# Optimization experiments

Measured on AMD Instinct MI355X. Metric: run time of the kernel, lower is better.

The kernel has to match this reference:

```python
import jax, jax.numpy as jnp
import numpy as np

N = 50000
EH = 500000
ES = 250000
D_IN = 128
D_HID = 128
N_CLS = 47


def _mean_agg(feat, src, dst, n):
    # gather src features, scatter-mean onto dst (DGL copy_u + mean)
    msg = feat[src]                                   # [E, d]
    s = jax.ops.segment_sum(msg, dst, num_segments=n)  # [N, d]
    cnt = jax.ops.segment_sum(jnp.ones((src.shape[0],), feat.dtype), dst, num_segments=n)
    return s / jnp.maximum(cnt, 1.0)[:, None]


def _sage_cv_layer(H, HBar, W, b, hs, hd, ss, sd):
    hbar_new = _mean_agg(HBar, hs, hd, N)             # history etype
    hdelta_new = _mean_agg(H - HBar, ss, sd, N)       # sampled etype
    h_neigh = hbar_new + hdelta_new
    z = jnp.concatenate([H, h_neigh], axis=1)         # [N, 2*d_in]
    return jax.nn.relu(z @ W.T + b)


def setup_inputs() -> dict:
    key = jax.random.key(0)
    ks = jax.random.split(key, 16)
    gain = float(np.sqrt(2.0))  # calculate_gain('relu')

    def xavier(k, shape):
        fan_out, fan_in = shape
        a = gain * np.sqrt(6.0 / (fan_in + fan_out))
        return jax.random.uniform(k, shape, jnp.float32, -a, a)

    return {
        "x": jax.random.normal(ks[0], (N, D_IN), jnp.float32),
        "hbar0": jax.random.normal(ks[1], (N, D_IN), jnp.float32),
        "hbar1": jax.random.normal(ks[2], (N, D_HID), jnp.float32),
        "W0": xavier(ks[3], (D_HID, 2 * D_IN)),
        "b0": jnp.zeros((D_HID,), jnp.float32),
        "W1": xavier(ks[4], (N_CLS, 2 * D_HID)),
        "b1": jnp.zeros((N_CLS,), jnp.float32),
        "hist_src0": jax.random.randint(ks[5], (EH,), 0, N),
        "hist_dst0": jax.random.randint(ks[6], (EH,), 0, N),
        "samp_src0": jax.random.randint(ks[7], (ES,), 0, N),
        "samp_dst0": jax.random.randint(ks[8], (ES,), 0, N),
        "hist_src1": jax.random.randint(ks[9], (EH,), 0, N),
        "hist_dst1": jax.random.randint(ks[10], (EH,), 0, N),
        "samp_src1": jax.random.randint(ks[11], (ES,), 0, N),
        "samp_dst1": jax.random.randint(ks[12], (ES,), 0, N),
    }


def reference(x, hbar0, hbar1, W0, b0, W1, b1,
              hist_src0, hist_dst0, samp_src0, samp_dst0,
              hist_src1, hist_dst1, samp_src1, samp_dst1):
    h = _sage_cv_layer(x, hbar0, W0, b0, hist_src0, hist_dst0, samp_src0, samp_dst0)
    h = _sage_cv_layer(h, hbar1, W1, b1, hist_src1, hist_dst1, samp_src1, samp_dst1)
    return h  # [N, n_classes]
```

## Files before the change

### kernel.cpp

```cpp
#include <hip/hip_runtime.h>

#define D_FEAT 128
#define K_DIM  256
#define EPB 4096
#define PADL 136


typedef __attribute__((ext_vector_type(8))) short bf16x8;
typedef __attribute__((ext_vector_type(4))) float f32x4;
typedef __attribute__((ext_vector_type(2))) float f32x2;

__device__ __forceinline__ unsigned short f2b(float f) {
    union { float f; unsigned u; } cv; cv.f = f;
    return (unsigned short)((cv.u + 0x7fffu + ((cv.u >> 16) & 1u)) >> 16);
}

__device__ __forceinline__ unsigned pack2(float lo, float hi) {
    return (unsigned)f2b(lo) | ((unsigned)f2b(hi) << 16);
}

__device__ __forceinline__ uint4 pack8(float4 a, float4 b) {
    return make_uint4(pack2(a.x, a.y), pack2(a.z, a.w), pack2(b.x, b.y), pack2(b.z, b.w));
}

__device__ __forceinline__ f32x2 up2(unsigned u) {
    union { unsigned u; float f; } lo, hi;
    lo.u = u << 16; hi.u = u & 0xffff0000u;
    f32x2 r; r.x = lo.f; r.y = hi.f; return r;
}

__device__ __forceinline__ void addu4p(f32x2* a, uint4 v) {
    a[0] += up2(v.x); a[1] += up2(v.y); a[2] += up2(v.z); a[3] += up2(v.w);
}

__device__ __forceinline__ float blo(unsigned u) { union { unsigned u; float f; } c; c.u = u << 16; return c.f; }
__device__ __forceinline__ float bhi(unsigned u) { union { unsigned u; float f; } c; c.u = u & 0xffff0000u; return c.f; }

__device__ __forceinline__ long yoff(int y, int EH, int ES) {
    return (long)((y + 1) >> 1) * EH + (long)(y >> 1) * ES;
}


__global__ __launch_bounds__(256)
void histB(const int* __restrict__ hd0, const int* __restrict__ sd0,
           const int* __restrict__ hd1, const int* __restrict__ sd1,
           int EH, int ES, int* __restrict__ bucketCnt, int nb2) {
    int y = blockIdx.y;
    const int* d = (y == 0) ? hd0 : (y == 1) ? sd0 : (y == 2) ? hd1 : sd1;
    int E = (y & 1) ? ES : EH;
    __shared__ int cnt[256];
    int t = threadIdx.x;
    cnt[t] = 0;
    __syncthreads();
    int i0 = blockIdx.x * EPB;
    #pragma unroll
    for (int j = 0; j < 16; ++j) {
        int i = i0 + j * 256 + t;
        if (i < E) atomicAdd(&cnt[d[i] >> 8], 1);
    }
    __syncthreads();
    if (t < nb2 && cnt[t] > 0) atomicAdd(&bucketCnt[y * nb2 + t], cnt[t]);
}

__global__ __launch_bounds__(256)
void scanBuckets(const int* __restrict__ bucketCnt, int* __restrict__ rpBucket,
                 int* __restrict__ bcur, int nb2) {
    int y = blockIdx.x;
    int t = threadIdx.x;
    __shared__ int sh[256];
    int c = (t < nb2) ? bucketCnt[y * nb2 + t] : 0;
    sh[t] = c;
    __syncthreads();
    for (int o = 1; o < 256; o <<= 1) {
        int x = (t >= o) ? sh[t - o] : 0;
        __syncthreads();
        sh[t] += x;
        __syncthreads();
    }
    int excl = t ? sh[t - 1] : 0;
    if (t < nb2) {
        rpBucket[y * (nb2 + 1) + t] = excl;
        bcur[y * nb2 + t] = excl;
    }
    if (t == 0) rpBucket[y * (nb2 + 1) + nb2] = sh[255];
}

__global__ __launch_bounds__(256)
void binA(const int* __restrict__ hs0, const int* __restrict__ hd0,
          const int* __restrict__ ss0, const int* __restrict__ sd0,
          const int* __restrict__ hs1, const int* __restrict__ hd1,
          const int* __restrict__ ss1, const int* __restrict__ sd1,
          int EH, int ES, int* __restrict__ bcur, unsigned* __restrict__ recs,
          int nb2) {
    int y = blockIdx.y;
    const int* src = (y == 0) ? hs0 : (y == 1) ? ss0 : (y == 2) ? hs1 : ss1;
    const int* dst = (y == 0) ? hd0 : (y == 1) ? sd0 : (y == 2) ? hd1 : sd1;
    int E = (y & 1) ? ES : EH;
    unsigned* rb = recs + yoff(y, EH, ES);

    __shared__ int cnt[256];
    int t = threadIdx.x;
    cnt[t] = 0;
    __syncthreads();
    int i0 = blockIdx.x * EPB;
    #pragma unroll
    for (int j = 0; j < 16; ++j) {
        int i = i0 + j * 256 + t;
        if (i < E) atomicAdd(&cnt[dst[i] >> 8], 1);
    }
    __syncthreads();
    int c = cnt[t];
    __syncthreads();
    if (t < nb2 && c > 0) cnt[t] = atomicAdd(&bcur[y * nb2 + t], c);
    __syncthreads();
    #pragma unroll
    for (int j = 0; j < 16; ++j) {
        int i = i0 + j * 256 + t;
        if (i < E) {
            int dd = dst[i];
            int slot = atomicAdd(&cnt[dd >> 8], 1);
            rb[slot] = (unsigned)src[i] | ((unsigned)(dd & 255) << 24);
        }
    }
}

__global__ __launch_bounds__(256)
void placeB(const unsigned* __restrict__ recs, const int* __restrict__ rpBucket,
            int* __restrict__ rpAll, int* __restrict__ srcAll,
            int EH, int ES, int n, int nb2) {
    int y = blockIdx.y;
    int b = blockIdx.x;
    int E = (y & 1) ? ES : EH;
    int* rp = rpAll + (size_t)y * (n + 1);
    long off = yoff(y, EH, ES);
    const unsigned* rb = recs + off;
    int* sb = srcAll + off;
    int e0 = rpBucket[y * (nb2 + 1) + b];
    int e1 = rpBucket[y * (nb2 + 1) + b + 1];
    int nodeBase = b << 8;

    __shared__ int cnt[256];
    __shared__ int sh[256];
    int t = threadIdx.x;
    cnt[t] = 0;
    __syncthreads();
    for (int e = e0 + t; e < e1; e += 256)
        atomicAdd(&cnt[rb[e] >> 24], 1);
    __syncthreads();
    sh[t] = cnt[t];
    __syncthreads();
    for (int o = 1; o < 256; o <<= 1) {
        int x = (t >= o) ? sh[t - o] : 0;
        __syncthreads();
        sh[t] += x;
        __syncthreads();
    }
    int base = e0 + (t ? sh[t - 1] : 0);
    if (nodeBase + t < n) rp[nodeBase + t] = base;
    if (b == 0 && t == 0) rp[n] = E;
    cnt[t] = base;
    __syncthreads();
    for (int e = e0 + t; e < e1; e += 256) {
        unsigned r = rb[e];
        int p = atomicAdd(&cnt[r >> 24], 1);
        sb[p] = (int)(r & 0x00FFFFFFu);
    }
}

__global__ __launch_bounds__(256)
void prep_static(const float4* __restrict__ x, const float4* __restrict__ hbar0,
                 const float4* __restrict__ hbar1,
                 uint4* __restrict__ hb0, uint4* __restrict__ db0,
                 uint4* __restrict__ hb1, uint4* __restrict__ z, int n16) {
    int i = blockIdx.x * 256 + threadIdx.x;
    if (i >= n16) return;
    float4 xa = x[i * 2],     xb = x[i * 2 + 1];
    float4 ba = hbar0[i * 2], bb = hbar0[i * 2 + 1];
    float4 ca = hbar1[i * 2], cb = hbar1[i * 2 + 1];
    hb0[i] = pack8(ba, bb);
    db0[i] = pack8(make_float4(xa.x - ba.x, xa.y - ba.y, xa.z - ba.z, xa.w - ba.w),
                   make_float4(xb.x - bb.x, xb.y - bb.y, xb.z - bb.z, xb.w - bb.w));
    hb1[i] = pack8(ca, cb);
    int g = i >> 4, seg = i & 15;
    int G = g >> 4, r = g & 15, k0 = seg >> 2, kq = seg & 3;
    z[((size_t)G * 8 + k0) * 64 + kq * 16 + r] = pack8(xa, xb);
}

__global__ __launch_bounds__(256)
void conv_weights(const float* __restrict__ W0, unsigned short* __restrict__ WbF0,
                  const float* __restrict__ W1, unsigned short* __restrict__ WbF1) {
    int i = blockIdx.x * 256 + threadIdx.x;
    if (i < 4096) {
        int k0 = i >> 9, T = (i >> 6) & 7, lane = i & 63;
        int col = T * 16 + (lane & 15);
        int kb = k0 * 32 + (lane >> 4) * 8;
        const float* src = W0 + (size_t)col * 256 + kb;
        unsigned short* dst = WbF0 + (size_t)i * 8;
        #pragma unroll
        for (int e = 0; e < 8; ++e) dst[e] = f2b(src[e]);
    }
    if (i < 1536) {
        int k0 = i / 192, rem = i % 192;
        int T = rem >> 6, lane = rem & 63;
        int col = T * 16 + (lane & 15);
        int kb = k0 * 32 + (lane >> 4) * 8;
        unsigned short* dst = WbF1 + (size_t)i * 8;
        #pragma unroll
        for (int e = 0; e < 8; ++e)
            dst[e] = (col < 47) ? f2b(W1[(size_t)col * 256 + kb + e]) : (unsigned short)0;
    }
}

__global__ __launch_bounds__(256)
void aggregate_z(const uint4* __restrict__ HB, const uint4* __restrict__ DB,
                 const int* __restrict__ rpH, const int* __restrict__ srcH,
                 const int* __restrict__ rpS, const int* __restrict__ srcS,
                 uint4* __restrict__ z, int n) {
    int g = blockIdx.x * 4 + (threadIdx.x >> 6);
    if (g >= n) return;
    int lane = threadIdx.x & 63;
    int j = lane >> 4, l = lane & 15;

    int hb_ = rpH[g], he = rpH[g + 1];
    int sb  = rpS[g], se = rpS[g + 1];
    int dH = he - hb_, dS = se - sb;
    int nIt = max((dH + 7) >> 3, (dS + 7) >> 3);

    f32x2 a[4] = {};
    f32x2 d[4] = {};

    int iH1 = hb_ + j, iH2 = hb_ + 4 + j;
    int iS1 = sb + j,  iS2 = sb + 4 + j;
    int sH1 = 0, sH2 = 0, sS1 = 0, sS2 = 0;
    if (iH1 < he) sH1 = srcH[iH1];
    if (iH2 < he) sH2 = srcH[iH2];
    if (iS1 < se) sS1 = srcS[iS1];
    if (iS2 < se) sS2 = srcS[iS2];

    for (int it = 0; it < nIt; ++it) {
        uint4 h1 = make_uint4(0, 0, 0, 0), h2 = make_uint4(0, 0, 0, 0);
        uint4 s1 = make_uint4(0, 0, 0, 0), s2 = make_uint4(0, 0, 0, 0);
        if (iH1 < he) h1 = HB[(size_t)sH1 * 16 + l];
        if (iH2 < he) h2 = HB[(size_t)sH2 * 16 + l];
        if (iS1 < se) s1 = DB[(size_t)sS1 * 16 + l];
        if (iS2 < se) s2 = DB[(size_t)sS2 * 16 + l];
        iH1 += 8; iH2 += 8; iS1 += 8; iS2 += 8;
        if (iH1 < he) sH1 = srcH[iH1];
        if (iH2 < he) sH2 = srcH[iH2];
        if (iS1 < se) sS1 = srcS[iS1];
        if (iS2 < se) sS2 = srcS[iS2];
        addu4p(a, h1); addu4p(a, h2);
        addu4p(d, s1); addu4p(d, s2);
    }

    float rH = 1.0f / fmaxf((float)dH, 1.0f);
    float rS = 1.0f / fmaxf((float)dS, 1.0f);
    float s[8];
    #pragma unroll
    for (int i = 0; i < 4; ++i) {
        float v0 = a[i].x * rH + d[i].x * rS;
        float v1 = a[i].y * rH + d[i].y * rS;
        v0 += __shfl_xor(v0, 16);
        v0 += __shfl_xor(v0, 32);
        v1 += __shfl_xor(v1, 16);
        v1 += __shfl_xor(v1, 32);
        s[2 * i] = v0;
        s[2 * i + 1] = v1;
    }
    if (j == 0) {
        uint4 rv = make_uint4(pack2(s[0], s[1]), pack2(s[2], s[3]),
                              pack2(s[4], s[5]), pack2(s[6], s[7]));
        size_t slot = ((size_t)(g >> 4) * 8 + 4 + (l >> 2)) * 64 + (l & 3) * 16 + (g & 15);
        z[slot] = rv;
    }
}

__global__ __launch_bounds__(256, 2)
void gemm_mfma_l0(const unsigned short* __restrict__ Z, const unsigned short* __restrict__ Wb,
                  const float* __restrict__ bias, const float* __restrict__ hbar1,
                  unsigned short* __restrict__ db1, unsigned short* __restrict__ zl, int n) {
    __shared__ unsigned short hl[32 * PADL];
    int tid  = threadIdx.x;
    int wave = tid >> 6;
    int lane = tid & 63;
    int rt = wave >> 1;
    int ch = wave & 1;
    int m0 = blockIdx.x * 32;
    int cl = lane & 15;
    int kq = lane >> 4;

    const short* Af = (const short*)Z;
    const short* Bf = (const short*)Wb;
    size_t G = (size_t)(m0 >> 4) + rt;

    bf16x8 aF[8];
    #pragma unroll
    for (int k0 = 0; k0 < 8; ++k0)
        aF[k0] = *(const bf16x8*)(Af + ((G * 8 + k0) * 64 + lane) * 8);

    f32x4 acc[4] = {};
    bf16x8 bF[2][4];
    #pragma unroll
    for (int t = 0; t < 4; ++t)
        bF[0][t] = *(const bf16x8*)(Bf + ((size_t)((0 * 8 + ch * 4 + t)) * 64 + lane) * 8);

    #pragma unroll
    for (int k0 = 0; k0 < 8; ++k0) {
        int cur = k0 & 1, nxt = cur ^ 1;
        if (k0 < 7) {
            #pragma unroll
            for (int t = 0; t < 4; ++t)
                bF[nxt][t] = *(const bf16x8*)(Bf + ((size_t)(((k0 + 1) * 8 + ch * 4 + t)) * 64 + lane) * 8);
        }
        #pragma unroll
        for (int t = 0; t < 4; ++t)
            acc[t] = __builtin_amdgcn_mfma_f32_16x16x32_bf16(aF[k0], bF[cur][t], acc[t], 0, 0, 0);
    }

    #pragma unroll
    for (int t = 0; t < 4; ++t) {
        int c = ch * 64 + t * 16 + cl;
        float bv = bias[c];
        #pragma unroll
        for (int r = 0; r < 4; ++r) {
            int row = rt * 16 + kq * 4 + r;
            hl[row * PADL + c] = f2b(fmaxf(acc[t][r] + bv, 0.0f));
        }
    }
    __syncthreads();

    #pragma unroll
    for (int s = 0; s < 2; ++s) {
        int ls = tid + s * 256;
        int gi = ls >> 8, k0 = (ls >> 6) & 3, ln = ls & 63;
        int rl = gi * 16 + (ln & 15);
        int col = k0 * 32 + (ln >> 4) * 8;
        int m = m0 + rl;
        if (m < n) {
            uint4 v = *(const uint4*)(hl + rl * PADL + col);
            ((uint4*)zl)[((size_t)(m0 >> 4) + gi) * 8 * 64 + (size_t)k0 * 64 + ln] = v;
        }
    }

    int row  = tid >> 3;
    int col  = (tid & 7) * 16;
    int m    = m0 + row;
    if (m < n) {
        const uint4* hr = (const uint4*)(hl + row * PADL + col);
        uint4 v0 = hr[0];
        uint4 v1 = hr[1];
        const float4* hb = (const float4*)(hbar1 + (size_t)m * 128 + col);
        float4 h0 = hb[0], h1 = hb[1], h2 = hb[2], h3 = hb[3];
        uint4 d0, d1;
        d0.x = pack2(blo(v0.x) - h0.x, bhi(v0.x) - h0.y);
        d0.y = pack2(blo(v0.y) - h0.z, bhi(v0.y) - h0.w);
        d0.z = pack2(blo(v0.z) - h1.x, bhi(v0.z) - h1.y);
        d0.w = pack2(blo(v0.w) - h1.z, bhi(v0.w) - h1.w);
        d1.x = pack2(blo(v1.x) - h2.x, bhi(v1.x) - h2.y);
        d1.y = pack2(blo(v1.y) - h2.z, bhi(v1.y) - h2.w);
        d1.z = pack2(blo(v1.z) - h3.x, bhi(v1.z) - h3.y);
        d1.w = pack2(blo(v1.w) - h3.z, bhi(v1.w) - h3.w);
        uint4* dp = (uint4*)(db1 + (size_t)m * 128 + col);
        dp[0] = d0;
        dp[1] = d1;
    }
}

template<int NT>
__global__ __launch_bounds__(128, 2)
void gemm_mfma(const unsigned short* __restrict__ Z, const unsigned short* __restrict__ Wb,
               const float* __restrict__ bias, float* __restrict__ out, int n, int COLS) {
    int wave = threadIdx.x >> 6;
    int lane = threadIdx.x & 63;
    int m0 = blockIdx.x * 32 + wave * 16;
    int cl = lane & 15;
    int kq = lane >> 4;

    const short* Af = (const short*)Z;
    const short* Bf = (const short*)Wb;
    size_t G = (size_t)(m0 >> 4);

    bf16x8 aF[8];
    #pragma unroll
    for (int k0 = 0; k0 < 8; ++k0)
        aF[k0] = *(const bf16x8*)(Af + ((G * 8 + k0) * 64 + lane) * 8);

    f32x4 acc[NT] = {};
    bf16x8 bF[2][NT];
    #pragma unroll
    for (int t = 0; t < NT; ++t)
        bF[0][t] = *(const bf16x8*)(Bf + ((size_t)(0 * NT + t) * 64 + lane) * 8);

    #pragma unroll
    for (int k0 = 0; k0 < 8; ++k0) {
        int cur = k0 & 1, nxt = cur ^ 1;
        if (k0 < 7) {
            #pragma unroll
            for (int t = 0; t < NT; ++t)
                bF[nxt][t] = *(const bf16x8*)(Bf + ((size_t)((k0 + 1) * NT + t) * 64 + lane) * 8);
        }
        #pragma unroll
        for (int t = 0; t < NT; ++t)
            acc[t] = __builtin_amdgcn_mfma_f32_16x16x32_bf16(aF[k0], bF[cur][t], acc[t], 0, 0, 0);
    }

    int rg = kq * 4;
    #pragma unroll
    for (int t = 0; t < NT; ++t) {
        int c = t * 16 + cl;
        if (c >= COLS) continue;
        float bv = bias[c];
        #pragma unroll
        for (int r = 0; r < 4; ++r) {
            int m = m0 + rg + r;
            if (m < n) out[(size_t)m * COLS + c] = fmaxf(acc[t][r] + bv, 0.f);
        }
    }
}

extern "C" void kernel_launch(void* const* d_in, const int* in_sizes, int n_in,
                              void* d_out, int out_size, void* d_ws, size_t ws_size,
                              hipStream_t stream) {
    const float* x     = (const float*)d_in[0];
    const float* hbar0 = (const float*)d_in[1];
    const float* hbar1 = (const float*)d_in[2];
    const float* W0    = (const float*)d_in[3];
    const float* b0    = (const float*)d_in[4];
    const float* W1    = (const float*)d_in[5];
    const float* b1    = (const float*)d_in[6];
    const int* hs0 = (const int*)d_in[7];
    const int* hd0 = (const int*)d_in[8];
    const int* ss0 = (const int*)d_in[9];
    const int* sd0 = (const int*)d_in[10];
    const int* hs1 = (const int*)d_in[11];
    const int* hd1 = (const int*)d_in[12];
    const int* ss1 = (const int*)d_in[13];
    const int* sd1 = (const int*)d_in[14];

    const int n   = in_sizes[0] / D_FEAT;
    const int EH  = in_sizes[7];
    const int ES  = in_sizes[9];
    const int nb2 = (n + 255) / 256;

    int* bucketCnt = (int*)d_ws;
    int* rpBucket  = bucketCnt + 4 * nb2;
    int* bcur      = rpBucket + 4 * (nb2 + 1);
    int* rpAll     = bcur + 4 * nb2;
    int* srcAll    = rpAll + 4 * (size_t)(n + 1);
    unsigned* recs = (unsigned*)(srcAll + 2 * (size_t)EH + 2 * (size_t)ES);
    size_t int_words = (size_t)12 * nb2 + 4 + 4 * (size_t)(n + 1)
                     + 4 * (size_t)EH + 4 * (size_t)ES;
    int_words = (int_words + 3) & ~(size_t)3;
    unsigned short* hb0 = (unsigned short*)((int*)d_ws + int_words);
    unsigned short* db0 = hb0 + (size_t)n * D_FEAT;
    unsigned short* hb1 = db0 + (size_t)n * D_FEAT;
    unsigned short* db1 = hb1 + (size_t)n * D_FEAT;
    unsigned short* z   = db1 + (size_t)n * D_FEAT;
    unsigned short* Wb0 = z + (size_t)n * K_DIM + 4096;
    unsigned short* Wb1 = Wb0 + 128 * 256;

    const int* rpH0 = rpAll;
    const int* rpS0 = rpAll + (size_t)(n + 1);
    const int* rpH1 = rpAll + 2 * (size_t)(n + 1);
    const int* rpS1 = rpAll + 3 * (size_t)(n + 1);
    int* srcH0 = srcAll;
    int* srcS0 = srcAll + (size_t)EH;
    int* srcH1 = srcAll + (size_t)EH + ES;
    int* srcS1 = srcAll + 2 * (size_t)EH + ES;

    dim3 blk(256);
    int binb  = (EH + EPB - 1) / EPB;
    int prepb = ((n * 16) + 255) / 256;
    int aggb  = (n + 3) / 4;
    int gemmb0 = (n + 31) / 32;
    int gemmb1 = (n + 31) / 32;

    hipMemsetAsync(bucketCnt, 0, 4 * (size_t)nb2 * sizeof(int), stream);
    conv_weights<<<16, blk, 0, stream>>>(W0, Wb0, W1, Wb1);
    histB<<<dim3(binb, 4), blk, 0, stream>>>(hd0, sd0, hd1, sd1, EH, ES, bucketCnt, nb2);
    scanBuckets<<<4, blk, 0, stream>>>(bucketCnt, rpBucket, bcur, nb2);
    binA<<<dim3(binb, 4), blk, 0, stream>>>(hs0, hd0, ss0, sd0, hs1, hd1, ss1, sd1,
                                            EH, ES, bcur, recs, nb2);
    placeB<<<dim3(nb2, 4), blk, 0, stream>>>(recs, rpBucket, rpAll, srcAll, EH, ES, n, nb2);
    prep_static<<<prepb, blk, 0, stream>>>((const float4*)x, (const float4*)hbar0,
                                           (const float4*)hbar1, (uint4*)hb0, (uint4*)db0,
                                           (uint4*)hb1, (uint4*)z, n * 16);

    aggregate_z<<<aggb, blk, 0, stream>>>((const uint4*)hb0, (const uint4*)db0,
                                          rpH0, srcH0, rpS0, srcS0, (uint4*)z, n);
    gemm_mfma_l0<<<gemmb0, blk, 0, stream>>>(z, Wb0, b0, hbar1, db1, z, n);

    aggregate_z<<<aggb, blk, 0, stream>>>((const uint4*)hb1, (const uint4*)db1,
                                          rpH1, srcH1, rpS1, srcS1, (uint4*)z, n);
    gemm_mfma<3><<<gemmb1, dim3(128), 0, stream>>>(z, Wb1, b1, (float*)d_out, n, 47);
}
```

Baseline: 300.5 us.

## Hoist layer-1 history aggregation into layer-0 aggregation launch

Layer 1's history-edge mean aggregation depends only on hbar1, not on layer 0's output. It is now computed in the same launch as layer 0's aggregation, using a second set of blocks, and written to a new bf16 buffer hm1. The layer-1 aggregation then gathers only sampled edges and adds hm1 in. History gathers also go 16 edges per iteration instead of 8 to increase memory-level parallelism. The trade-off is an extra intermediate buffer write and read, plus an extra bf16 rounding of the history mean.

Result: slower. 315.1 us (+4.9%).

```diff
diff --git a/kernel.cpp b/kernel.cpp
--- a/kernel.cpp
+++ b/kernel.cpp
@@ -212,54 +212,166 @@
 }
 
 __global__ __launch_bounds__(256)
-void aggregate_z(const uint4* __restrict__ HB, const uint4* __restrict__ DB,
-                 const int* __restrict__ rpH, const int* __restrict__ srcH,
-                 const int* __restrict__ rpS, const int* __restrict__ srcS,
-                 uint4* __restrict__ z, int n) {
+void agg_l0_h1(const uint4* __restrict__ HB0, const uint4* __restrict__ DB0,
+               const int* __restrict__ rpH0, const int* __restrict__ srcH0,
+               const int* __restrict__ rpS0, const int* __restrict__ srcS0,
+               uint4* __restrict__ z,
+               const uint4* __restrict__ HB1, const int* __restrict__ rpH1,
+               const int* __restrict__ srcH1, uint4* __restrict__ hm1,
+               int n, int nblk0) {
+    int lane = threadIdx.x & 63;
+    int j = lane >> 4, l = lane & 15;
+
+    if ((int)blockIdx.x < nblk0) {
+        int g = blockIdx.x * 4 + (threadIdx.x >> 6);
+        if (g >= n) return;
+        int hb_ = rpH0[g], he = rpH0[g + 1];
+        int sb  = rpS0[g], se = rpS0[g + 1];
+        int dH = he - hb_, dS = se - sb;
+        int nH = (dH + 15) >> 4, nS = (dS + 7) >> 3;
+        int nIt = nH > nS ? nH : nS;
+
+        f32x2 a[4] = {};
+        f32x2 d[4] = {};
+
+        int iH1 = hb_ + j, iH2 = hb_ + 4 + j, iH3 = hb_ + 8 + j, iH4 = hb_ + 12 + j;
+        int iS1 = sb + j,  iS2 = sb + 4 + j;
+        int sH1 = 0, sH2 = 0, sH3 = 0, sH4 = 0, sS1 = 0, sS2 = 0;
+        if (iH1 < he) sH1 = srcH0[iH1];
+        if (iH2 < he) sH2 = srcH0[iH2];
+        if (iH3 < he) sH3 = srcH0[iH3];
+        if (iH4 < he) sH4 = srcH0[iH4];
+        if (iS1 < se) sS1 = srcS0[iS1];
+        if (iS2 < se) sS2 = srcS0[iS2];
+
+        for (int it = 0; it < nIt; ++it) {
+            uint4 h1 = make_uint4(0,0,0,0), h2 = make_uint4(0,0,0,0);
+            uint4 h3 = make_uint4(0,0,0,0), h4 = make_uint4(0,0,0,0);
+            uint4 s1 = make_uint4(0,0,0,0), s2 = make_uint4(0,0,0,0);
+            if (iH1 < he) h1 = HB0[(size_t)sH1 * 16 + l];
+            if (iH2 < he) h2 = HB0[(size_t)sH2 * 16 + l];
+            if (iH3 < he) h3 = HB0[(size_t)sH3 * 16 + l];
+            if (iH4 < he) h4 = HB0[(size_t)sH4 * 16 + l];
+            if (iS1 < se) s1 = DB0[(size_t)sS1 * 16 + l];
+            if (iS2 < se) s2 = DB0[(size_t)sS2 * 16 + l];
+            iH1 += 16; iH2 += 16; iH3 += 16; iH4 += 16;
+            iS1 += 8;  iS2 += 8;
+            if (iH1 < he) sH1 = srcH0[iH1];
+            if (iH2 < he) sH2 = srcH0[iH2];
+            if (iH3 < he) sH3 = srcH0[iH3];
+            if (iH4 < he) sH4 = srcH0[iH4];
+            if (iS1 < se) sS1 = srcS0[iS1];
+            if (iS2 < se) sS2 = srcS0[iS2];
+            addu4p(a, h1); addu4p(a, h2); addu4p(a, h3); addu4p(a, h4);
+            addu4p(d, s1); addu4p(d, s2);
+        }
+
+        float rH = 1.0f / fmaxf((float)dH, 1.0f);
+        float rS = 1.0f / fmaxf((float)dS, 1.0f);
+        float s[8];
+        #pragma unroll
+        for (int i = 0; i < 4; ++i) {
+            float v0 = a[i].x * rH + d[i].x * rS;
+            float v1 = a[i].y * rH + d[i].y * rS;
+            v0 += __shfl_xor(v0, 16);
+            v0 += __shfl_xor(v0, 32);
+            v1 += __shfl_xor(v1, 16);
+            v1 += __shfl_xor(v1, 32);
+            s[2 * i] = v0;
+            s[2 * i + 1] = v1;
+        }
+        if (j == 0) {
+            uint4 rv = make_uint4(pack2(s[0], s[1]), pack2(s[2], s[3]),
+                                  pack2(s[4], s[5]), pack2(s[6], s[7]));
+            size_t slot = ((size_t)(g >> 4) * 8 + 4 + (l >> 2)) * 64 + (l & 3) * 16 + (g & 15);
+            z[slot] = rv;
+        }
+    } else {
+        int g = ((int)blockIdx.x - nblk0) * 4 + (threadIdx.x >> 6);
+        if (g >= n) return;
+        int hb_ = rpH1[g], he = rpH1[g + 1];
+        int dH = he - hb_;
+        int nIt = (dH + 15) >> 4;
+
+        f32x2 a[4] = {};
+        int iH1 = hb_ + j, iH2 = hb_ + 4 + j, iH3 = hb_ + 8 + j, iH4 = hb_ + 12 + j;
+        int sH1 = 0, sH2 = 0, sH3 = 0, sH4 = 0;
+        if (iH1 < he) sH1 = srcH1[iH1];
+        if (iH2 < he) sH2 = srcH1[iH2];
+        if (iH3 < he) sH3 = srcH1[iH3];
+        if (iH4 < he) sH4 = srcH1[iH4];
+
+        for (int it = 0; it < nIt; ++it) {
+            uint4 h1 = make_uint4(0,0,0,0), h2 = make_uint4(0,0,0,0);
+            uint4 h3 = make_uint4(0,0,0,0), h4 = make_uint4(0,0,0,0);
+            if (iH1 < he) h1 = HB1[(size_t)sH1 * 16 + l];
+            if (iH2 < he) h2 = HB1[(size_t)sH2 * 16 + l];
+            if (iH3 < he) h3 = HB1[(size_t)sH3 * 16 + l];
+            if (iH4 < he) h4 = HB1[(size_t)sH4 * 16 + l];
+            iH1 += 16; iH2 += 16; iH3 += 16; iH4 += 16;
+            if (iH1 < he) sH1 = srcH1[iH1];
+            if (iH2 < he) sH2 = srcH1[iH2];
+            if (iH3 < he) sH3 = srcH1[iH3];
+            if (iH4 < he) sH4 = srcH1[iH4];
+            addu4p(a, h1); addu4p(a, h2); addu4p(a, h3); addu4p(a, h4);
+        }
+
+        float rH = 1.0f / fmaxf((float)dH, 1.0f);
+        float s[8];
+        #pragma unroll
+        for (int i = 0; i < 4; ++i) {
+            float v0 = a[i].x * rH;
+            float v1 = a[i].y * rH;
+            v0 += __shfl_xor(v0, 16);
+            v0 += __shfl_xor(v0, 32);
+            v1 += __shfl_xor(v1, 16);
+            v1 += __shfl_xor(v1, 32);
+            s[2 * i] = v0;
+            s[2 * i + 1] = v1;
+        }
+        if (j == 0) {
+            uint4 rv = make_uint4(pack2(s[0], s[1]), pack2(s[2], s[3]),
+                                  pack2(s[4], s[5]), pack2(s[6], s[7]));
+            hm1[(size_t)g * 16 + l] = rv;
+        }
+    }
+}
+
+__global__ __launch_bounds__(256)
+void agg_s1(const uint4* __restrict__ DB1, const int* __restrict__ rpS,
+            const int* __restrict__ srcS, const uint4* __restrict__ hm1,
+            uint4* __restrict__ z, int n) {
     int g = blockIdx.x * 4 + (threadIdx.x >> 6);
     if (g >= n) return;
     int lane = threadIdx.x & 63;
     int j = lane >> 4, l = lane & 15;
 
-    int hb_ = rpH[g], he = rpH[g + 1];
-    int sb  = rpS[g], se = rpS[g + 1];
-    int dH = he - hb_, dS = se - sb;
-    int nIt = max((dH + 7) >> 3, (dS + 7) >> 3);
-
-    f32x2 a[4] = {};
+    int sb = rpS[g], se = rpS[g + 1];
+    int dS = se - sb;
+    int nIt = (dS + 7) >> 3;
+
     f32x2 d[4] = {};
-
-    int iH1 = hb_ + j, iH2 = hb_ + 4 + j;
-    int iS1 = sb + j,  iS2 = sb + 4 + j;
-    int sH1 = 0, sH2 = 0, sS1 = 0, sS2 = 0;
-    if (iH1 < he) sH1 = srcH[iH1];
-    if (iH2 < he) sH2 = srcH[iH2];
+    int iS1 = sb + j, iS2 = sb + 4 + j;
+    int sS1 = 0, sS2 = 0;
     if (iS1 < se) sS1 = srcS[iS1];
     if (iS2 < se) sS2 = srcS[iS2];
 
     for (int it = 0; it < nIt; ++it) {
-        uint4 h1 = make_uint4(0, 0, 0, 0), h2 = make_uint4(0, 0, 0, 0);
-        uint4 s1 = make_uint4(0, 0, 0, 0), s2 = make_uint4(0, 0, 0, 0);
-        if (iH1 < he) h1 = HB[(size_t)sH1 * 16 + l];
-        if (iH2 < he) h2 = HB[(size_t)sH2 * 16 + l];
-        if (iS1 < se) s1 = DB[(size_t)sS1 * 16 + l];
-        if (iS2 < se) s2 = DB[(size_t)sS2 * 16 + l];
-        iH1 += 8; iH2 += 8; iS1 += 8; iS2 += 8;
-        if (iH1 < he) sH1 = srcH[iH1];
-        if (iH2 < he) sH2 = srcH[iH2];
+        uint4 s1 = make_uint4(0,0,0,0), s2 = make_uint4(0,0,0,0);
+        if (iS1 < se) s1 = DB1[(size_t)sS1 * 16 + l];
+        if (iS2 < se) s2 = DB1[(size_t)sS2 * 16 + l];
+        iS1 += 8; iS2 += 8;
         if (iS1 < se) sS1 = srcS[iS1];
         if (iS2 < se) sS2 = srcS[iS2];
-        addu4p(a, h1); addu4p(a, h2);
         addu4p(d, s1); addu4p(d, s2);
     }
 
-    float rH = 1.0f / fmaxf((float)dH, 1.0f);
     float rS = 1.0f / fmaxf((float)dS, 1.0f);
     float s[8];
     #pragma unroll
     for (int i = 0; i < 4; ++i) {
-        float v0 = a[i].x * rH + d[i].x * rS;
-        float v1 = a[i].y * rH + d[i].y * rS;
+        float v0 = d[i].x * rS;
+        float v1 = d[i].y * rS;
         v0 += __shfl_xor(v0, 16);
         v0 += __shfl_xor(v0, 32);
         v1 += __shfl_xor(v1, 16);
@@ -268,6 +380,11 @@
         s[2 * i + 1] = v1;
     }
     if (j == 0) {
+        uint4 hm = hm1[(size_t)g * 16 + l];
+        s[0] += blo(hm.x); s[1] += bhi(hm.x);
+        s[2] += blo(hm.y); s[3] += bhi(hm.y);
+        s[4] += blo(hm.z); s[5] += bhi(hm.z);
+        s[6] += blo(hm.w); s[7] += bhi(hm.w);
         uint4 rv = make_uint4(pack2(s[0], s[1]), pack2(s[2], s[3]),
                               pack2(s[4], s[5]), pack2(s[6], s[7]));
         size_t slot = ((size_t)(g >> 4) * 8 + 4 + (l >> 2)) * 64 + (l & 3) * 16 + (g & 15);
@@ -458,6 +575,7 @@
     unsigned short* z   = db1 + (size_t)n * D_FEAT;
     unsigned short* Wb0 = z + (size_t)n * K_DIM + 4096;
     unsigned short* Wb1 = Wb0 + 128 * 256;
+    unsigned short* hm1 = Wb1 + 64 * 256;
 
     const int* rpH0 = rpAll;
     const int* rpS0 = rpAll + (size_t)(n + 1);
@@ -486,11 +604,13 @@
                                            (const float4*)hbar1, (uint4*)hb0, (uint4*)db0,
                                            (uint4*)hb1, (uint4*)z, n * 16);
 
-    aggregate_z<<<aggb, blk, 0, stream>>>((const uint4*)hb0, (const uint4*)db0,
-                                          rpH0, srcH0, rpS0, srcS0, (uint4*)z, n);
+    agg_l0_h1<<<2 * aggb, blk, 0, stream>>>((const uint4*)hb0, (const uint4*)db0,
+                                            rpH0, srcH0, rpS0, srcS0, (uint4*)z,
+                                            (const uint4*)hb1, rpH1, srcH1, (uint4*)hm1,
+                                            n, aggb);
     gemm_mfma_l0<<<gemmb0, blk, 0, stream>>>(z, Wb0, b0, hbar1, db1, z, n);
 
-    aggregate_z<<<aggb, blk, 0, stream>>>((const uint4*)hb1, (const uint4*)db1,
-                                          rpH1, srcH1, rpS1, srcS1, (uint4*)z, n);
+    agg_s1<<<aggb, blk, 0, stream>>>((const uint4*)db1, rpS1, srcS1, (const uint4*)hm1,
+                                     (uint4*)z, n);
     gemm_mfma<3><<<gemmb1, dim3(128), 0, stream>>>(z, Wb1, b1, (float*)d_out, n, 47);
 }
```

## Replace two-level bucket CSR build with per-node global-atomic counting sort

Applied to the files above, without the earlier changes.

Replaces the bucketed histogram/bin/place CSR construction with a direct per-node count using global atomics, a two-level scan (per-block, then across blocks), a base fix-up, and a single scatter pass with global atomic cursors. It also fuses feature prep, weight conversion and the degree histogram into one launch. The aim is fewer kernel launches and no intermediate packed-record pass. In exchange it relies on contended global atomics, and the edge order within a node's list is no longer deterministic.

Result: slower. 395.2 us (+31.5%).

```diff
diff --git a/kernel.cpp b/kernel.cpp
--- a/kernel.cpp
+++ b/kernel.cpp
@@ -40,174 +40,137 @@
     return (long)((y + 1) >> 1) * EH + (long)(y >> 1) * ES;
 }
 
-
-__global__ __launch_bounds__(256)
-void histB(const int* __restrict__ hd0, const int* __restrict__ sd0,
-           const int* __restrict__ hd1, const int* __restrict__ sd1,
-           int EH, int ES, int* __restrict__ bucketCnt, int nb2) {
-    int y = blockIdx.y;
-    const int* d = (y == 0) ? hd0 : (y == 1) ? sd0 : (y == 2) ? hd1 : sd1;
-    int E = (y & 1) ? ES : EH;
-    __shared__ int cnt[256];
+__global__ __launch_bounds__(256)
+void head(const float4* __restrict__ x, const float4* __restrict__ hbar0,
+          const float4* __restrict__ hbar1,
+          uint4* __restrict__ hb0, uint4* __restrict__ db0,
+          uint4* __restrict__ hb1, uint4* __restrict__ z, int n16,
+          const float* __restrict__ W0, unsigned short* __restrict__ WbF0,
+          const float* __restrict__ W1, unsigned short* __restrict__ WbF1,
+          const int* __restrict__ hd0, const int* __restrict__ sd0,
+          const int* __restrict__ hd1, const int* __restrict__ sd1,
+          int EH, int ES, int* __restrict__ cnt, int n, int prepb, int binb) {
+    int bid = blockIdx.x;
     int t = threadIdx.x;
-    cnt[t] = 0;
-    __syncthreads();
-    int i0 = blockIdx.x * EPB;
-    #pragma unroll
-    for (int j = 0; j < 16; ++j) {
-        int i = i0 + j * 256 + t;
-        if (i < E) atomicAdd(&cnt[d[i] >> 8], 1);
-    }
-    __syncthreads();
-    if (t < nb2 && cnt[t] > 0) atomicAdd(&bucketCnt[y * nb2 + t], cnt[t]);
-}
-
-__global__ __launch_bounds__(256)
-void scanBuckets(const int* __restrict__ bucketCnt, int* __restrict__ rpBucket,
-                 int* __restrict__ bcur, int nb2) {
-    int y = blockIdx.x;
-    int t = threadIdx.x;
+    if (bid < prepb) {
+        int i = bid * 256 + t;
+        if (i >= n16) return;
+        float4 xa = x[i * 2],     xb = x[i * 2 + 1];
+        float4 ba = hbar0[i * 2], bb = hbar0[i * 2 + 1];
+        float4 ca = hbar1[i * 2], cb = hbar1[i * 2 + 1];
+        hb0[i] = pack8(ba, bb);
+        db0[i] = pack8(make_float4(xa.x - ba.x, xa.y - ba.y, xa.z - ba.z, xa.w - ba.w),
+                       make_float4(xb.x - bb.x, xb.y - bb.y, xb.z - bb.z, xb.w - bb.w));
+        hb1[i] = pack8(ca, cb);
+        int g = i >> 4, seg = i & 15;
+        int G = g >> 4, r = g & 15, k0 = seg >> 2, kq = seg & 3;
+        z[((size_t)G * 8 + k0) * 64 + kq * 16 + r] = pack8(xa, xb);
+    } else if (bid < prepb + 16) {
+        int i = (bid - prepb) * 256 + t;
+        if (i < 4096) {
+            int k0 = i >> 9, T = (i >> 6) & 7, lane = i & 63;
+            int col = T * 16 + (lane & 15);
+            int kb = k0 * 32 + (lane >> 4) * 8;
+            const float* src = W0 + (size_t)col * 256 + kb;
+            unsigned short* dst = WbF0 + (size_t)i * 8;
+            #pragma unroll
+            for (int e = 0; e < 8; ++e) dst[e] = f2b(src[e]);
+        }
+        if (i < 1536) {
+            int k0 = i / 192, rem = i % 192;
+            int T = rem >> 6, lane = rem & 63;
+            int col = T * 16 + (lane & 15);
+            int kb = k0 * 32 + (lane >> 4) * 8;
+            unsigned short* dst = WbF1 + (size_t)i * 8;
+            #pragma unroll
+            for (int e = 0; e < 8; ++e)
+                dst[e] = (col < 47) ? f2b(W1[(size_t)col * 256 + kb + e]) : (unsigned short)0;
+        }
+    } else {
+        int r = bid - prepb - 16;
+        int y = r / binb, c = r % binb;
+        const int* d = (y == 0) ? hd0 : (y == 1) ? sd0 : (y == 2) ? hd1 : sd1;
+        int E = (y & 1) ? ES : EH;
+        int* cn = cnt + (size_t)y * n;
+        int i0 = c * EPB;
+        #pragma unroll
+        for (int j = 0; j < 16; ++j) {
+            int i = i0 + j * 256 + t;
+            if (i < E) atomicAdd(&cn[d[i]], 1);
+        }
+    }
+}
+
+__global__ __launch_bounds__(256)
+void scanN(const int* __restrict__ cnt, int* __restrict__ rpAll,
+           int* __restrict__ bucketSum, int n, int nb2) {
+    int y = blockIdx.y, b = blockIdx.x, t = threadIdx.x;
+    int node = b * 256 + t;
     __shared__ int sh[256];
-    int c = (t < nb2) ? bucketCnt[y * nb2 + t] : 0;
+    int c = (node < n) ? cnt[(size_t)y * n + node] : 0;
     sh[t] = c;
     __syncthreads();
     for (int o = 1; o < 256; o <<= 1) {
-        int x = (t >= o) ? sh[t - o] : 0;
+        int v = (t >= o) ? sh[t - o] : 0;
         __syncthreads();
-        sh[t] += x;
+        sh[t] += v;
         __syncthreads();
     }
-    int excl = t ? sh[t - 1] : 0;
-    if (t < nb2) {
-        rpBucket[y * (nb2 + 1) + t] = excl;
-        bcur[y * nb2 + t] = excl;
-    }
-    if (t == 0) rpBucket[y * (nb2 + 1) + nb2] = sh[255];
-}
-
-__global__ __launch_bounds__(256)
-void binA(const int* __restrict__ hs0, const int* __restrict__ hd0,
-          const int* __restrict__ ss0, const int* __restrict__ sd0,
-          const int* __restrict__ hs1, const int* __restrict__ hd1,
-          const int* __restrict__ ss1, const int* __restrict__ sd1,
-          int EH, int ES, int* __restrict__ bcur, unsigned* __restrict__ recs,
-          int nb2) {
+    if (node < n) rpAll[(size_t)y * (n + 1) + node] = sh[t] - c;
+    if (t == 255) bucketSum[y * nb2 + b] = sh[255];
+}
+
+__global__ __launch_bounds__(256)
+void scanB(const int* __restrict__ bucketSum, int* __restrict__ rpBucket, int nb2) {
+    int y = blockIdx.x, t = threadIdx.x;
+    __shared__ int sh[256];
+    int c = (t < nb2) ? bucketSum[y * nb2 + t] : 0;
+    sh[t] = c;
+    __syncthreads();
+    for (int o = 1; o < 256; o <<= 1) {
+        int v = (t >= o) ? sh[t - o] : 0;
+        __syncthreads();
+        sh[t] += v;
+        __syncthreads();
+    }
+    if (t < nb2) rpBucket[y * (nb2 + 1) + t] = sh[t] - c;
+}
+
+__global__ __launch_bounds__(256)
+void baseFix(int* __restrict__ rpAll, int* __restrict__ cur,
+             const int* __restrict__ rpBucket, int n, int nb2, int EH, int ES) {
+    int y = blockIdx.y;
+    int node = blockIdx.x * 256 + threadIdx.x;
+    if (node < n) {
+        int v = rpAll[(size_t)y * (n + 1) + node] + rpBucket[y * (nb2 + 1) + (node >> 8)];
+        rpAll[(size_t)y * (n + 1) + node] = v;
+        cur[(size_t)y * n + node] = v;
+    }
+    if (blockIdx.x == 0 && threadIdx.x == 0)
+        rpAll[(size_t)y * (n + 1) + n] = (y & 1) ? ES : EH;
+}
+
+__global__ __launch_bounds__(256)
+void scatterE(const int* __restrict__ hs0, const int* __restrict__ hd0,
+              const int* __restrict__ ss0, const int* __restrict__ sd0,
+              const int* __restrict__ hs1, const int* __restrict__ hd1,
+              const int* __restrict__ ss1, const int* __restrict__ sd1,
+              int EH, int ES, int* __restrict__ cur, int* __restrict__ srcAll, int n) {
     int y = blockIdx.y;
     const int* src = (y == 0) ? hs0 : (y == 1) ? ss0 : (y == 2) ? hs1 : ss1;
     const int* dst = (y == 0) ? hd0 : (y == 1) ? sd0 : (y == 2) ? hd1 : sd1;
     int E = (y & 1) ? ES : EH;
-    unsigned* rb = recs + yoff(y, EH, ES);
-
-    __shared__ int cnt[256];
+    int* cn = cur + (size_t)y * n;
+    int* sb = srcAll + yoff(y, EH, ES);
     int t = threadIdx.x;
-    cnt[t] = 0;
-    __syncthreads();
     int i0 = blockIdx.x * EPB;
-    #pragma unroll
-    for (int j = 0; j < 16; ++j) {
-        int i = i0 + j * 256 + t;
-        if (i < E) atomicAdd(&cnt[dst[i] >> 8], 1);
-    }
-    __syncthreads();
-    int c = cnt[t];
-    __syncthreads();
-    if (t < nb2 && c > 0) cnt[t] = atomicAdd(&bcur[y * nb2 + t], c);
-    __syncthreads();
     #pragma unroll
     for (int j = 0; j < 16; ++j) {
         int i = i0 + j * 256 + t;
         if (i < E) {
-            int dd = dst[i];
-            int slot = atomicAdd(&cnt[dd >> 8], 1);
-            rb[slot] = (unsigned)src[i] | ((unsigned)(dd & 255) << 24);
-        }
-    }
-}
-
-__global__ __launch_bounds__(256)
-void placeB(const unsigned* __restrict__ recs, const int* __restrict__ rpBucket,
-            int* __restrict__ rpAll, int* __restrict__ srcAll,
-            int EH, int ES, int n, int nb2) {
-    int y = blockIdx.y;
-    int b = blockIdx.x;
-    int E = (y & 1) ? ES : EH;
-    int* rp = rpAll + (size_t)y * (n + 1);
-    long off = yoff(y, EH, ES);
-    const unsigned* rb = recs + off;
-    int* sb = srcAll + off;
-    int e0 = rpBucket[y * (nb2 + 1) + b];
-    int e1 = rpBucket[y * (nb2 + 1) + b + 1];
-    int nodeBase = b << 8;
-
-    __shared__ int cnt[256];
-    __shared__ int sh[256];
-    int t = threadIdx.x;
-    cnt[t] = 0;
-    __syncthreads();
-    for (int e = e0 + t; e < e1; e += 256)
-        atomicAdd(&cnt[rb[e] >> 24], 1);
-    __syncthreads();
-    sh[t] = cnt[t];
-    __syncthreads();
-    for (int o = 1; o < 256; o <<= 1) {
-        int x = (t >= o) ? sh[t - o] : 0;
-        __syncthreads();
-        sh[t] += x;
-        __syncthreads();
-    }
-    int base = e0 + (t ? sh[t - 1] : 0);
-    if (nodeBase + t < n) rp[nodeBase + t] = base;
-    if (b == 0 && t == 0) rp[n] = E;
-    cnt[t] = base;
-    __syncthreads();
-    for (int e = e0 + t; e < e1; e += 256) {
-        unsigned r = rb[e];
-        int p = atomicAdd(&cnt[r >> 24], 1);
-        sb[p] = (int)(r & 0x00FFFFFFu);
-    }
-}
-
-__global__ __launch_bounds__(256)
-void prep_static(const float4* __restrict__ x, const float4* __restrict__ hbar0,
-                 const float4* __restrict__ hbar1,
-                 uint4* __restrict__ hb0, uint4* __restrict__ db0,
-                 uint4* __restrict__ hb1, uint4* __restrict__ z, int n16) {
-    int i = blockIdx.x * 256 + threadIdx.x;
-    if (i >= n16) return;
-    float4 xa = x[i * 2],     xb = x[i * 2 + 1];
-    float4 ba = hbar0[i * 2], bb = hbar0[i * 2 + 1];
-    float4 ca = hbar1[i * 2], cb = hbar1[i * 2 + 1];
-    hb0[i] = pack8(ba, bb);
-    db0[i] = pack8(make_float4(xa.x - ba.x, xa.y - ba.y, xa.z - ba.z, xa.w - ba.w),
-                   make_float4(xb.x - bb.x, xb.y - bb.y, xb.z - bb.z, xb.w - bb.w));
-    hb1[i] = pack8(ca, cb);
-    int g = i >> 4, seg = i & 15;
-    int G = g >> 4, r = g & 15, k0 = seg >> 2, kq = seg & 3;
-    z[((size_t)G * 8 + k0) * 64 + kq * 16 + r] = pack8(xa, xb);
-}
-
-__global__ __launch_bounds__(256)
-void conv_weights(const float* __restrict__ W0, unsigned short* __restrict__ WbF0,
-                  const float* __restrict__ W1, unsigned short* __restrict__ WbF1) {
-    int i = blockIdx.x * 256 + threadIdx.x;
-    if (i < 4096) {
-        int k0 = i >> 9, T = (i >> 6) & 7, lane = i & 63;
-        int col = T * 16 + (lane & 15);
-        int kb = k0 * 32 + (lane >> 4) * 8;
-        const float* src = W0 + (size_t)col * 256 + kb;
-        unsigned short* dst = WbF0 + (size_t)i * 8;
-        #pragma unroll
-        for (int e = 0; e < 8; ++e) dst[e] = f2b(src[e]);
-    }
-    if (i < 1536) {
-        int k0 = i / 192, rem = i % 192;
-        int T = rem >> 6, lane = rem & 63;
-        int col = T * 16 + (lane & 15);
-        int kb = k0 * 32 + (lane >> 4) * 8;
-        unsigned short* dst = WbF1 + (size_t)i * 8;
-        #pragma unroll
-        for (int e = 0; e < 8; ++e)
-            dst[e] = (col < 47) ? f2b(W1[(size_t)col * 256 + kb + e]) : (unsigned short)0;
+            int slot = atomicAdd(&cn[dst[i]], 1);
+            sb[slot] = src[i];
+        }
     }
 }
 
@@ -442,14 +405,14 @@
     const int ES  = in_sizes[9];
     const int nb2 = (n + 255) / 256;
 
-    int* bucketCnt = (int*)d_ws;
-    int* rpBucket  = bucketCnt + 4 * nb2;
-    int* bcur      = rpBucket + 4 * (nb2 + 1);
-    int* rpAll     = bcur + 4 * nb2;
+    int* cnt       = (int*)d_ws;
+    int* cur       = cnt + 4 * (size_t)n;
+    int* bucketSum = cur + 4 * (size_t)n;
+    int* rpBucket  = bucketSum + 4 * nb2;
+    int* rpAll     = rpBucket + 4 * (nb2 + 1);
     int* srcAll    = rpAll + 4 * (size_t)(n + 1);
-    unsigned* recs = (unsigned*)(srcAll + 2 * (size_t)EH + 2 * (size_t)ES);
-    size_t int_words = (size_t)12 * nb2 + 4 + 4 * (size_t)(n + 1)
-                     + 4 * (size_t)EH + 4 * (size_t)ES;
+    size_t int_words = 8 * (size_t)n + 4 * nb2 + 4 * (nb2 + 1) + 4 * (size_t)(n + 1)
+                     + 2 * (size_t)EH + 2 * (size_t)ES;
     int_words = (int_words + 3) & ~(size_t)3;
     unsigned short* hb0 = (unsigned short*)((int*)d_ws + int_words);
     unsigned short* db0 = hb0 + (size_t)n * D_FEAT;
@@ -475,16 +438,16 @@
     int gemmb0 = (n + 31) / 32;
     int gemmb1 = (n + 31) / 32;
 
-    hipMemsetAsync(bucketCnt, 0, 4 * (size_t)nb2 * sizeof(int), stream);
-    conv_weights<<<16, blk, 0, stream>>>(W0, Wb0, W1, Wb1);
-    histB<<<dim3(binb, 4), blk, 0, stream>>>(hd0, sd0, hd1, sd1, EH, ES, bucketCnt, nb2);
-    scanBuckets<<<4, blk, 0, stream>>>(bucketCnt, rpBucket, bcur, nb2);
-    binA<<<dim3(binb, 4), blk, 0, stream>>>(hs0, hd0, ss0, sd0, hs1, hd1, ss1, sd1,
-                                            EH, ES, bcur, recs, nb2);
-    placeB<<<dim3(nb2, 4), blk, 0, stream>>>(recs, rpBucket, rpAll, srcAll, EH, ES, n, nb2);
-    prep_static<<<prepb, blk, 0, stream>>>((const float4*)x, (const float4*)hbar0,
-                                           (const float4*)hbar1, (uint4*)hb0, (uint4*)db0,
-                                           (uint4*)hb1, (uint4*)z, n * 16);
+    hipMemsetAsync(cnt, 0, 4 * (size_t)n * sizeof(int), stream);
+    head<<<prepb + 16 + 4 * binb, blk, 0, stream>>>(
+        (const float4*)x, (const float4*)hbar0, (const float4*)hbar1,
+        (uint4*)hb0, (uint4*)db0, (uint4*)hb1, (uint4*)z, n * 16,
+        W0, Wb0, W1, Wb1, hd0, sd0, hd1, sd1, EH, ES, cnt, n, prepb, binb);
+    scanN<<<dim3(nb2, 4), blk, 0, stream>>>(cnt, rpAll, bucketSum, n, nb2);
+    scanB<<<4, blk, 0, stream>>>(bucketSum, rpBucket, nb2);
+    baseFix<<<dim3(nb2, 4), blk, 0, stream>>>(rpAll, cur, rpBucket, n, nb2, EH, ES);
+    scatterE<<<dim3(binb, 4), blk, 0, stream>>>(hs0, hd0, ss0, sd0, hs1, hd1, ss1, sd1,
+                                                EH, ES, cur, srcAll, n);
 
     aggregate_z<<<aggb, blk, 0, stream>>>((const uint4*)hb0, (const uint4*)db0,
                                           rpH0, srcH0, rpS0, srcS0, (uint4*)z, n);
```

## Merge binning, feature prep and weight conversion into one launch; cache bucket records in LDS

Applied to the files above, without the earlier changes.

Combines binA, prep_static and conv_weights into a single heterogeneous kernel that dispatches work by block index, removing two launches and letting the memory-bound prep work overlap with edge binning. placeB now keeps each bucket's records in a 16KB shared buffer during the counting pass and reads them back from there when scattering, so the second global read of the records is avoided. The extra shared memory in placeB may lower occupancy, and buckets with more than PB_CAP records still read the overflow from global memory.

New measurement: 291.9 us. 1.03x faster.

```diff
diff --git a/kernel.cpp b/kernel.cpp
--- a/kernel.cpp
+++ b/kernel.cpp
@@ -4,6 +4,7 @@
 #define K_DIM  256
 #define EPB 4096
 #define PADL 136
+#define PB_CAP 4096
 
 
 typedef __attribute__((ext_vector_type(8))) short bf16x8;
@@ -86,40 +87,84 @@
 }
 
 __global__ __launch_bounds__(256)
-void binA(const int* __restrict__ hs0, const int* __restrict__ hd0,
-          const int* __restrict__ ss0, const int* __restrict__ sd0,
-          const int* __restrict__ hs1, const int* __restrict__ hd1,
-          const int* __restrict__ ss1, const int* __restrict__ sd1,
-          int EH, int ES, int* __restrict__ bcur, unsigned* __restrict__ recs,
-          int nb2) {
-    int y = blockIdx.y;
-    const int* src = (y == 0) ? hs0 : (y == 1) ? ss0 : (y == 2) ? hs1 : ss1;
-    const int* dst = (y == 0) ? hd0 : (y == 1) ? sd0 : (y == 2) ? hd1 : sd1;
-    int E = (y & 1) ? ES : EH;
-    unsigned* rb = recs + yoff(y, EH, ES);
-
+void binPrep(const int* __restrict__ hs0, const int* __restrict__ hd0,
+             const int* __restrict__ ss0, const int* __restrict__ sd0,
+             const int* __restrict__ hs1, const int* __restrict__ hd1,
+             const int* __restrict__ ss1, const int* __restrict__ sd1,
+             int EH, int ES, int* __restrict__ bcur, unsigned* __restrict__ recs,
+             int nb2, int binb,
+             const float4* __restrict__ x, const float4* __restrict__ hbar0,
+             const float4* __restrict__ hbar1,
+             uint4* __restrict__ hb0, uint4* __restrict__ db0,
+             uint4* __restrict__ hb1, uint4* __restrict__ z, int n16, int prepb,
+             const float* __restrict__ W0, unsigned short* __restrict__ WbF0,
+             const float* __restrict__ W1, unsigned short* __restrict__ WbF1) {
     __shared__ int cnt[256];
+    int bid = blockIdx.x;
     int t = threadIdx.x;
-    cnt[t] = 0;
-    __syncthreads();
-    int i0 = blockIdx.x * EPB;
-    #pragma unroll
-    for (int j = 0; j < 16; ++j) {
-        int i = i0 + j * 256 + t;
-        if (i < E) atomicAdd(&cnt[dst[i] >> 8], 1);
-    }
-    __syncthreads();
-    int c = cnt[t];
-    __syncthreads();
-    if (t < nb2 && c > 0) cnt[t] = atomicAdd(&bcur[y * nb2 + t], c);
-    __syncthreads();
-    #pragma unroll
-    for (int j = 0; j < 16; ++j) {
-        int i = i0 + j * 256 + t;
-        if (i < E) {
-            int dd = dst[i];
-            int slot = atomicAdd(&cnt[dd >> 8], 1);
-            rb[slot] = (unsigned)src[i] | ((unsigned)(dd & 255) << 24);
+
+    if (bid < 4 * binb) {
+        int y = bid / binb, c = bid % binb;
+        const int* src = (y == 0) ? hs0 : (y == 1) ? ss0 : (y == 2) ? hs1 : ss1;
+        const int* dst = (y == 0) ? hd0 : (y == 1) ? sd0 : (y == 2) ? hd1 : sd1;
+        int E = (y & 1) ? ES : EH;
+        unsigned* rb = recs + yoff(y, EH, ES);
+
+        cnt[t] = 0;
+        __syncthreads();
+        int i0 = c * EPB;
+        #pragma unroll
+        for (int j = 0; j < 16; ++j) {
+            int i = i0 + j * 256 + t;
+            if (i < E) atomicAdd(&cnt[dst[i] >> 8], 1);
+        }
+        __syncthreads();
+        int cc = cnt[t];
+        __syncthreads();
+        if (t < nb2 && cc > 0) cnt[t] = atomicAdd(&bcur[y * nb2 + t], cc);
+        __syncthreads();
+        #pragma unroll
+        for (int j = 0; j < 16; ++j) {
+            int i = i0 + j * 256 + t;
+            if (i < E) {
+                int dd = dst[i];
+                int slot = atomicAdd(&cnt[dd >> 8], 1);
+                rb[slot] = (unsigned)src[i] | ((unsigned)(dd & 255) << 24);
+            }
+        }
+    } else if (bid < 4 * binb + prepb) {
+        int i = (bid - 4 * binb) * 256 + t;
+        if (i >= n16) return;
+        float4 xa = x[i * 2],     xb = x[i * 2 + 1];
+        float4 ba = hbar0[i * 2], bb = hbar0[i * 2 + 1];
+        float4 ca = hbar1[i * 2], cb = hbar1[i * 2 + 1];
+        hb0[i] = pack8(ba, bb);
+        db0[i] = pack8(make_float4(xa.x - ba.x, xa.y - ba.y, xa.z - ba.z, xa.w - ba.w),
+                       make_float4(xb.x - bb.x, xb.y - bb.y, xb.z - bb.z, xb.w - bb.w));
+        hb1[i] = pack8(ca, cb);
+        int g = i >> 4, seg = i & 15;
+        int G = g >> 4, r = g & 15, k0 = seg >> 2, kq = seg & 3;
+        z[((size_t)G * 8 + k0) * 64 + kq * 16 + r] = pack8(xa, xb);
+    } else {
+        int i = (bid - 4 * binb - prepb) * 256 + t;
+        if (i < 4096) {
+            int k0 = i >> 9, T = (i >> 6) & 7, lane = i & 63;
+            int col = T * 16 + (lane & 15);
+            int kb = k0 * 32 + (lane >> 4) * 8;
+            const float* src = W0 + (size_t)col * 256 + kb;
+            unsigned short* dst = WbF0 + (size_t)i * 8;
+            #pragma unroll
+            for (int e = 0; e < 8; ++e) dst[e] = f2b(src[e]);
+        }
+        if (i < 1536) {
+            int k0 = i / 192, rem = i % 192;
+            int T = rem >> 6, lane = rem & 63;
+            int col = T * 16 + (lane & 15);
+            int kb = k0 * 32 + (lane >> 4) * 8;
+            unsigned short* dst = WbF1 + (size_t)i * 8;
+            #pragma unroll
+            for (int e = 0; e < 8; ++e)
+                dst[e] = (col < 47) ? f2b(W1[(size_t)col * 256 + kb + e]) : (unsigned short)0;
         }
     }
 }
@@ -138,21 +183,26 @@
     int e0 = rpBucket[y * (nb2 + 1) + b];
     int e1 = rpBucket[y * (nb2 + 1) + b + 1];
     int nodeBase = b << 8;
-
+    int ne = e1 - e0;
+
+    __shared__ unsigned eb[PB_CAP];
     __shared__ int cnt[256];
     __shared__ int sh[256];
     int t = threadIdx.x;
     cnt[t] = 0;
     __syncthreads();
-    for (int e = e0 + t; e < e1; e += 256)
-        atomicAdd(&cnt[rb[e] >> 24], 1);
+    for (int e = t; e < ne; e += 256) {
+        unsigned r = rb[e0 + e];
+        if (e < PB_CAP) eb[e] = r;
+        atomicAdd(&cnt[r >> 24], 1);
+    }
     __syncthreads();
     sh[t] = cnt[t];
     __syncthreads();
     for (int o = 1; o < 256; o <<= 1) {
-        int x = (t >= o) ? sh[t - o] : 0;
-        __syncthreads();
-        sh[t] += x;
+        int v = (t >= o) ? sh[t - o] : 0;
+        __syncthreads();
+        sh[t] += v;
         __syncthreads();
     }
     int base = e0 + (t ? sh[t - 1] : 0);
@@ -160,54 +210,10 @@
     if (b == 0 && t == 0) rp[n] = E;
     cnt[t] = base;
     __syncthreads();
-    for (int e = e0 + t; e < e1; e += 256) {
-        unsigned r = rb[e];
+    for (int e = t; e < ne; e += 256) {
+        unsigned r = (e < PB_CAP) ? eb[e] : rb[e0 + e];
         int p = atomicAdd(&cnt[r >> 24], 1);
         sb[p] = (int)(r & 0x00FFFFFFu);
-    }
-}
-
-__global__ __launch_bounds__(256)
-void prep_static(const float4* __restrict__ x, const float4* __restrict__ hbar0,
-                 const float4* __restrict__ hbar1,
-                 uint4* __restrict__ hb0, uint4* __restrict__ db0,
-                 uint4* __restrict__ hb1, uint4* __restrict__ z, int n16) {
-    int i = blockIdx.x * 256 + threadIdx.x;
-    if (i >= n16) return;
-    float4 xa = x[i * 2],     xb = x[i * 2 + 1];
-    float4 ba = hbar0[i * 2], bb = hbar0[i * 2 + 1];
-    float4 ca = hbar1[i * 2], cb = hbar1[i * 2 + 1];
-    hb0[i] = pack8(ba, bb);
-    db0[i] = pack8(make_float4(xa.x - ba.x, xa.y - ba.y, xa.z - ba.z, xa.w - ba.w),
-                   make_float4(xb.x - bb.x, xb.y - bb.y, xb.z - bb.z, xb.w - bb.w));
-    hb1[i] = pack8(ca, cb);
-    int g = i >> 4, seg = i & 15;
-    int G = g >> 4, r = g & 15, k0 = seg >> 2, kq = seg & 3;
-    z[((size_t)G * 8 + k0) * 64 + kq * 16 + r] = pack8(xa, xb);
-}
-
-__global__ __launch_bounds__(256)
-void conv_weights(const float* __restrict__ W0, unsigned short* __restrict__ WbF0,
-                  const float* __restrict__ W1, unsigned short* __restrict__ WbF1) {
-    int i = blockIdx.x * 256 + threadIdx.x;
-    if (i < 4096) {
-        int k0 = i >> 9, T = (i >> 6) & 7, lane = i & 63;
-        int col = T * 16 + (lane & 15);
-        int kb = k0 * 32 + (lane >> 4) * 8;
-        const float* src = W0 + (size_t)col * 256 + kb;
-        unsigned short* dst = WbF0 + (size_t)i * 8;
-        #pragma unroll
-        for (int e = 0; e < 8; ++e) dst[e] = f2b(src[e]);
-    }
-    if (i < 1536) {
-        int k0 = i / 192, rem = i % 192;
-        int T = rem >> 6, lane = rem & 63;
-        int col = T * 16 + (lane & 15);
-        int kb = k0 * 32 + (lane >> 4) * 8;
-        unsigned short* dst = WbF1 + (size_t)i * 8;
-        #pragma unroll
-        for (int e = 0; e < 8; ++e)
-            dst[e] = (col < 47) ? f2b(W1[(size_t)col * 256 + kb + e]) : (unsigned short)0;
     }
 }
 
@@ -476,15 +482,14 @@
     int gemmb1 = (n + 31) / 32;
 
     hipMemsetAsync(bucketCnt, 0, 4 * (size_t)nb2 * sizeof(int), stream);
-    conv_weights<<<16, blk, 0, stream>>>(W0, Wb0, W1, Wb1);
     histB<<<dim3(binb, 4), blk, 0, stream>>>(hd0, sd0, hd1, sd1, EH, ES, bucketCnt, nb2);
     scanBuckets<<<4, blk, 0, stream>>>(bucketCnt, rpBucket, bcur, nb2);
-    binA<<<dim3(binb, 4), blk, 0, stream>>>(hs0, hd0, ss0, sd0, hs1, hd1, ss1, sd1,
-                                            EH, ES, bcur, recs, nb2);
+    binPrep<<<4 * binb + prepb + 16, blk, 0, stream>>>(
+        hs0, hd0, ss0, sd0, hs1, hd1, ss1, sd1, EH, ES, bcur, recs, nb2, binb,
+        (const float4*)x, (const float4*)hbar0, (const float4*)hbar1,
+        (uint4*)hb0, (uint4*)db0, (uint4*)hb1, (uint4*)z, n * 16, prepb,
+        W0, Wb0, W1, Wb1);
     placeB<<<dim3(nb2, 4), blk, 0, stream>>>(recs, rpBucket, rpAll, srcAll, EH, ES, n, nb2);
-    prep_static<<<prepb, blk, 0, stream>>>((const float4*)x, (const float4*)hbar0,
-                                           (const float4*)hbar1, (uint4*)hb0, (uint4*)db0,
-                                           (uint4*)hb1, (uint4*)z, n * 16);
 
     aggregate_z<<<aggb, blk, 0, stream>>>((const uint4*)hb0, (const uint4*)db0,
                                           rpH0, srcH0, rpS0, srcS0, (uint4*)z, n);
```
